# Kernel optimization log

Hardware: AMD Instinct MI355X
Metric: run time of the kernel (lower is better)

## Reference

```python
import jax, jax.numpy as jnp
import numpy as np

DEPTH, C, HS, NH, WS, B = 10, 128, 512, 8, 2, 4096


def _sincos_1d(embed_dim, pos):
    omega = np.arange(embed_dim // 2, dtype=np.float64)
    omega /= embed_dim / 2.0
    omega = 1.0 / 10000 ** omega
    out = np.einsum('m,d->md', pos.reshape(-1), omega)
    return np.concatenate([np.sin(out), np.cos(out)], axis=1)


def _sincos_pos_embed(embed_dim, grid_size):
    g = np.arange(grid_size, dtype=np.float32)
    grid = np.stack(np.meshgrid(g, g), axis=0).reshape(2, -1)
    emb_h = _sincos_1d(embed_dim // 2, grid[0])
    emb_w = _sincos_1d(embed_dim // 2, grid[1])
    return np.concatenate([emb_h, emb_w], axis=1)  # (16, HS)


def _encode_board(x):
    # x: (B,128) int piece ids -> (B,12,8,8) one-hot planes (vectorized encodeBoard)
    x = x.reshape(-1, 2, 8, 8)
    pieces = jnp.arange(1, 7)
    white = (x[:, 0, None, :, :] == pieces[None, :, None, None]).astype(jnp.float32)
    black = (x[:, 1, None, :, :] == pieces[None, :, None, None]).astype(jnp.float32)
    return jnp.concatenate([white, black], axis=1)


def _conv3x3(x, w, b):
    y = jax.lax.conv_general_dilated(x, w, (1, 1), 'SAME',
                                     dimension_numbers=('NCHW', 'OIHW', 'NCHW'))
    return y + b[None, :, None, None]


def _bn(x, g, b, eps=1e-5):
    # training-mode BatchNorm2d: per-batch stats over (N,H,W)
    m = x.mean((0, 2, 3), keepdims=True)
    v = x.var((0, 2, 3), keepdims=True)
    return (x - m) * jax.lax.rsqrt(v + eps) * g[None, :, None, None] + b[None, :, None, None]


def _ln(x, eps=1e-6):
    m = x.mean(-1, keepdims=True)
    v = x.var(-1, keepdims=True)
    return (x - m) * jax.lax.rsqrt(v + eps)


def _window_partition(x, ws):
    b, c, h, w = x.shape
    x = x.reshape(b, c, h // ws, ws, w // ws, ws)
    x = x.transpose(0, 2, 4, 3, 5, 1)  # b h w p1 p2 c
    return x.reshape(b, (h // ws) * (w // ws), ws * ws * c)


def _window_reverse(win, ws, h, w):
    b, n, d = win.shape
    c = d // (ws * ws)
    x = win.reshape(b, h // ws, w // ws, ws, ws, c)
    x = x.transpose(0, 5, 1, 3, 2, 4)  # b c h p1 w p2
    return x.reshape(b, c, h, w)


def _attention(t, qkv_w, qkv_b, proj_w, proj_b):
    b, n, d = t.shape
    hd = d // NH
    qkv = (t @ qkv_w + qkv_b).reshape(b, n, 3, NH, hd)
    q, k, v = jnp.moveaxis(qkv, 2, 0)  # each (b,n,NH,hd)
    attn = jax.nn.softmax(jnp.einsum('bqhd,bkhd->bhqk', q * hd ** -0.5, k), axis=-1)
    out = jnp.einsum('bhqk,bkhd->bqhd', attn, v).reshape(b, n, d)
    return out @ proj_w + proj_b


def _block(x, pos, p):
    (rb1_w, rb1_b, g1, b1, rb2_w, rb2_b, g2, b2,
     qkv_w, qkv_b, proj_w, proj_b, f1_w, f1_b, f2_w, f2_b) = p
    h, w = x.shape[2], x.shape[3]
    z = _bn(_conv3x3(jax.nn.relu(x), rb1_w, rb1_b), g1, b1)
    z = _bn(_conv3x3(jax.nn.relu(z), rb2_w, rb2_b), g2, b2)
    x = x + z
    t = _window_partition(x, WS) + pos
    t = t + _ln(_attention(t, qkv_w, qkv_b, proj_w, proj_b))
    t = t + _ln(jax.nn.relu(t @ f1_w + f1_b) @ f2_w + f2_b)
    return _window_reverse(t, WS, h, w)


def _forward(x, pos_embed, conv1_w, conv1_b, blk, lin1_w, lin1_b, lin2_w, lin2_b):
    h = _conv3x3(_encode_board(x), conv1_w, conv1_b)

    def step(h, p):
        return _block(h, pos_embed, p), None

    h, _ = jax.lax.scan(step, h, blk)
    feat = h.transpose(0, 2, 3, 1).reshape(h.shape[0], -1)  # B (H W C)
    logits = jax.nn.relu(feat @ lin1_w + lin1_b) @ lin2_w + lin2_b
    return jax.nn.softmax(logits, axis=1)


def setup_inputs() -> dict:
    key = jax.random.key(0)
    ks = jax.random.split(key, 16)
    n = lambda k, shp: jax.random.normal(k, shp, dtype=jnp.float32) * 0.02
    inp = {}
    inp['x'] = jax.random.randint(ks[0], (B, 128), 0, 7)
    inp['pos_embed'] = jnp.asarray(_sincos_pos_embed(HS, 8 // WS), dtype=jnp.float32)[None]
    inp['conv1_w'] = n(ks[1], (C, 12, 3, 3))
    inp['conv1_b'] = jnp.zeros((C,), jnp.float32)
    inp['rb1_w'] = n(ks[2], (DEPTH, C, C, 3, 3)); inp['rb1_b'] = jnp.zeros((DEPTH, C), jnp.float32)
    inp['bn1_g'] = jnp.ones((DEPTH, C), jnp.float32); inp['bn1_b'] = jnp.zeros((DEPTH, C), jnp.float32)
    inp['rb2_w'] = n(ks[3], (DEPTH, C, C, 3, 3)); inp['rb2_b'] = jnp.zeros((DEPTH, C), jnp.float32)
    inp['bn2_g'] = jnp.ones((DEPTH, C), jnp.float32); inp['bn2_b'] = jnp.zeros((DEPTH, C), jnp.float32)
    inp['qkv_w'] = n(ks[4], (DEPTH, HS, 3 * HS)); inp['qkv_b'] = jnp.zeros((DEPTH, 3 * HS), jnp.float32)
    inp['proj_w'] = n(ks[5], (DEPTH, HS, HS)); inp['proj_b'] = jnp.zeros((DEPTH, HS), jnp.float32)
    inp['fc1_w'] = n(ks[6], (DEPTH, HS, HS)); inp['fc1_b'] = jnp.zeros((DEPTH, HS), jnp.float32)
    inp['fc2_w'] = n(ks[7], (DEPTH, HS, HS)); inp['fc2_b'] = jnp.zeros((DEPTH, HS), jnp.float32)
    inp['lin1_w'] = n(ks[8], (C * 64, 1024)); inp['lin1_b'] = jnp.zeros((1024,), jnp.float32)
    inp['lin2_w'] = n(ks[9], (1024, 640)); inp['lin2_b'] = jnp.zeros((640,), jnp.float32)
    return inp


def reference(x, pos_embed, conv1_w, conv1_b, rb1_w, rb1_b, bn1_g, bn1_b,
              rb2_w, rb2_b, bn2_g, bn2_b, qkv_w, qkv_b, proj_w, proj_b,
              fc1_w, fc1_b, fc2_w, fc2_b, lin1_w, lin1_b, lin2_w, lin2_b):
    blk = (rb1_w, rb1_b, bn1_g, bn1_b, rb2_w, rb2_b, bn2_g, bn2_b,
           qkv_w, qkv_b, proj_w, proj_b, fc1_w, fc1_b, fc2_w, fc2_b)
    return _forward(x, pos_embed, conv1_w, conv1_b, blk, lin1_w, lin1_b, lin2_w, lin2_b)
```

## Files before the change

### kernel.cpp

```cpp
#include <hip/hip_runtime.h>
#include <hip/hip_fp16.h>
#include <math.h>


#define NBATCH 4096
#define NPOSR  (NBATCH*64)
#define CH     1024
#define CHT    (CH*16)

#define OFF_ACT   0
#define OFF_BIG2  33554432
#define OFF_WT1   (OFF_BIG2 + 16777216)
#define OFF_WTA   (OFF_WT1 + 13824)
#define OFF_WTB   (OFF_WTA + 737280)
#define OFF_WTT   (OFF_WTB + 737280)
#define OFF_STATS (OFF_WTT + 786432)
#define OFF_BIAS  (OFF_STATS + 5120)
#define WS_NEED_FLOATS (OFF_BIAS + 1536)

#define H_QKVB 0
#define H_ATT  25165824
#define H_T2H  8388608
#define H_LOG  8388608

#define T_QKV  0
#define T_PRJ  786432
#define T_F1   1048576
#define T_F2   1310720

typedef _Float16 f16x8 __attribute__((ext_vector_type(8)));
typedef _Float16 f16x4 __attribute__((ext_vector_type(4)));
typedef float f32x4 __attribute__((ext_vector_type(4)));

__device__ inline f32x4 vzero4() { f32x4 z; z[0]=0.f; z[1]=0.f; z[2]=0.f; z[3]=0.f; return z; }

__device__ inline float4 ld_half4(const __half* p) {
  float2 a = __half22float2(*(const __half2*)p);
  float2 b = __half22float2(*(const __half2*)(p + 2));
  return make_float4(a.x, a.y, b.x, b.y);
}

__device__ __forceinline__ void gll16(const void* g, void* lds) {
  __builtin_amdgcn_global_load_lds(
      (__attribute__((address_space(1))) void*)g,
      (__attribute__((address_space(3))) void*)lds,
      16, 0, 0);
}

__global__ void k_zero(float* __restrict__ s) { s[blockIdx.x*256 + threadIdx.x] = 0.f; }

__global__ void k_sentinel(float* __restrict__ out, int n, float val) {
  for (int i = blockIdx.x*blockDim.x + threadIdx.x; i < n; i += gridDim.x*blockDim.x)
    out[i] = val;
}

__global__ __launch_bounds__(256) void k_cvt16(const float* __restrict__ src,
    __half* __restrict__ dst, int n8) {
  int i = blockIdx.x*blockDim.x + threadIdx.x;
  if (i >= n8) return;
  const float4* s4 = (const float4*)&src[i*8];
  float4 v0 = s4[0], v1 = s4[1];
  f16x8 h;
  h[0]=(_Float16)v0.x; h[1]=(_Float16)v0.y; h[2]=(_Float16)v0.z; h[3]=(_Float16)v0.w;
  h[4]=(_Float16)v1.x; h[5]=(_Float16)v1.y; h[6]=(_Float16)v1.z; h[7]=(_Float16)v1.w;
  *(f16x8*)&dst[i*8] = h;
}

__global__ void k_wprep(const float* __restrict__ src, float* __restrict__ dst, int L, int Cin) {
  int total = L * 128 * Cin * 9;
  for (int idx = blockIdx.x*blockDim.x + threadIdx.x; idx < total; idx += gridDim.x*blockDim.x) {
    int kk = idx % 9; int t2 = idx / 9;
    int ci = t2 % Cin; t2 /= Cin;
    int co = t2 % 128; int l  = t2 / 128;
    dst[((size_t)(l*9 + kk)*Cin + ci)*128 + co] = src[idx];
  }
}

__global__ void k_wprep16(const float* __restrict__ src, __half* __restrict__ dst, int L) {
  int total = L * 128 * 128 * 9;
  for (int idx = blockIdx.x*blockDim.x + threadIdx.x; idx < total; idx += gridDim.x*blockDim.x) {
    int kk = idx % 9; int t2 = idx / 9;
    int ci = t2 % 128; t2 /= 128;
    int co = t2 % 128; int l  = t2 / 128;
    dst[((size_t)(l*128 + co))*1152 + kk*128 + ci] = __float2half(src[idx]);
  }
}

__global__ void k_wt16(const float* __restrict__ W, __half* __restrict__ WT, int K, int N) {
  int total = K * N;
  for (int idx = blockIdx.x*blockDim.x + threadIdx.x; idx < total; idx += gridDim.x*blockDim.x) {
    int k = idx / N, n = idx % N;
    WT[(size_t)n*K + k] = __float2half(W[idx]);
  }
}

__global__ void k_wt16x4(const float* __restrict__ Wq, const float* __restrict__ Wp,
                         const float* __restrict__ W1, const float* __restrict__ W2,
                         const float* __restrict__ bq,
                         __half* __restrict__ wTt, float* __restrict__ biasbuf) {
  int gid0 = blockIdx.x*blockDim.x + threadIdx.x;
  if (gid0 < 1536) biasbuf[gid0] = bq[gid0] * (gid0 < 512 ? 0.125f : 1.f);
  const int TOT = 786432 + 3*262144;
  for (int idx = gid0; idx < TOT; idx += gridDim.x*blockDim.x) {
    if (idx < 786432) {
      int k = idx / 1536, n = idx % 1536;
      float v = Wq[idx] * (n < 512 ? 0.125f : 1.f);
      wTt[T_QKV + (size_t)n*512 + k] = __float2half(v);
    } else {
      int r0 = idx - 786432;
      int s = r0 / 262144, r = r0 % 262144;
      int k = r / 512, n = r % 512;
      const float* W = (s == 0) ? Wp : (s == 1) ? W1 : W2;
      wTt[T_PRJ + s*262144 + (size_t)n*512 + k] = __float2half(W[r]);
    }
  }
}

__global__ __launch_bounds__(256) void k_conv1(const int* __restrict__ xin,
    const float* __restrict__ wT1, const float* __restrict__ b1,
    float* __restrict__ out) {
  __shared__ int s_w[64], s_b[64];
  int b = blockIdx.x, t = threadIdx.x;
  if (t < 64) { s_w[t] = xin[b*128 + t]; s_b[t] = xin[b*128 + 64 + t]; }
  __syncthreads();
  int p = t >> 2, i = t & 3;
  int y = p >> 3, x = p & 7;
  float acc[32];
  #pragma unroll
  for (int j = 0; j < 32; ++j) acc[j] = b1[i*32 + j];
  #pragma unroll
  for (int kk = 0; kk < 9; ++kk) {
    int ny = y + kk/3 - 1, nx = x + kk%3 - 1;
    if (ny < 0 || ny > 7 || nx < 0 || nx > 7) continue;
    int np = ny*8 + nx;
    int wp = s_w[np], bp = s_b[np];
    if (wp >= 1 && wp <= 6) {
      const float* w = &wT1[(size_t)(kk*12 + (wp-1))*128 + i*32];
      #pragma unroll
      for (int j = 0; j < 32; ++j) acc[j] += w[j];
    }
    if (bp >= 1 && bp <= 6) {
      const float* w = &wT1[(size_t)(kk*12 + 6 + (bp-1))*128 + i*32];
      #pragma unroll
      for (int j = 0; j < 32; ++j) acc[j] += w[j];
    }
  }
  float* o = &out[((size_t)b*64 + p)*128 + i*32];
  #pragma unroll
  for (int j = 0; j < 8; ++j)
    *(float4*)&o[j*4] = make_float4(acc[j*4], acc[j*4+1], acc[j*4+2], acc[j*4+3]);
}

__device__ inline float cvt_in(float v) { return v; }
__device__ inline float cvt_in(__half v) { return __half2float(v); }

#define IMG_W 136

template<typename TIN>
__global__ __launch_bounds__(256) void k_conv_mfma(const TIN* __restrict__ in,
    const __half* __restrict__ wT , const float* __restrict__ bias,
    const float* __restrict__ stats_in, const float* __restrict__ g,
    const float* __restrict__ bb, int use_bn, __half* __restrict__ out,
    float* __restrict__ stats_out) {
  __shared__ __align__(16) _Float16 s_img[2*65*IMG_W];
  __shared__ __align__(16) _Float16 s_B[2][4096];
  __shared__ float s_sum[128], s_sq[128];
  __shared__ float s_bnp[256];
  int b2 = blockIdx.x, t = threadIdx.x;
  int w = t >> 6, lane = t & 63;

  auto issueB = [&](int win, int buf) {
    #pragma unroll
    for (int i = 0; i < 2; ++i) {
      int rbase = (w*2 + i)*16;
      const __half* g2 = &wT[(size_t)(rbase + (lane>>2))*1152 + win*32 + (lane&3)*8];
      gll16(g2, &s_B[buf][rbase*32]);
    }
  };
  issueB(0, 0);

  if (use_bn && t < 128) {
    const float invN = 1.f / (float)NPOSR;
    float m = stats_in[t] * invN;
    float vv = stats_in[128+t] * invN - m*m;
    float sc = g[t] * rsqrtf(vv + 1e-5f);
    s_bnp[t] = sc;
    s_bnp[128+t] = bb[t] - m*sc;
  }
  __syncthreads();

  for (int idx4 = t; idx4 < 4096; idx4 += 256) {
    int img = idx4 >> 11, rr = (idx4 >> 5) & 63, c4 = (idx4 & 31) * 4;
    const TIN* src = &in[((size_t)(b2*2 + img)*64 + rr)*128 + c4];
    float v0 = cvt_in(src[0]), v1 = cvt_in(src[1]), v2 = cvt_in(src[2]), v3 = cvt_in(src[3]);
    if (use_bn) {
      v0 = s_bnp[c4+0]*v0 + s_bnp[128+c4+0];
      v1 = s_bnp[c4+1]*v1 + s_bnp[128+c4+1];
      v2 = s_bnp[c4+2]*v2 + s_bnp[128+c4+2];
      v3 = s_bnp[c4+3]*v3 + s_bnp[128+c4+3];
    }
    f16x4 h;
    h[0] = (_Float16)fmaxf(v0, 0.f); h[1] = (_Float16)fmaxf(v1, 0.f);
    h[2] = (_Float16)fmaxf(v2, 0.f); h[3] = (_Float16)fmaxf(v3, 0.f);
    *(f16x4*)&s_img[(img*65 + rr)*IMG_W + c4] = h;
  }
  {
    int img = t >> 7, c = t & 127;
    s_img[(img*65 + 64)*IMG_W + c] = (_Float16)0.f;
    if (t < 128) { s_sum[t] = 0.f; s_sq[t] = 0.f; }
  }
  int wm = (w >> 1)*64, wn = (w & 1)*64;
  int fr = lane & 15, fq = lane >> 4;
  int imgo[4], yy[4], xx_[4];
  #pragma unroll
  for (int mt = 0; mt < 4; ++mt) {
    int r = wm + mt*16 + fr;
    imgo[mt] = r >> 6; int p = r & 63; yy[mt] = p >> 3; xx_[mt] = p & 7;
  }
  f32x4 acc[4][4];
  #pragma unroll
  for (int mt = 0; mt < 4; ++mt)
    #pragma unroll
    for (int nt = 0; nt < 4; ++nt) acc[mt][nt] = vzero4();
  __syncthreads();

  #pragma unroll
  for (int kk = 0; kk < 9; ++kk) {
    int dy = kk/3 - 1, dx = kk%3 - 1;
    const _Float16* abase[4];
    #pragma unroll
    for (int mt = 0; mt < 4; ++mt) {
      int ny = yy[mt] + dy, nx = xx_[mt] + dx;
      int row = ((unsigned)ny < 8u && (unsigned)nx < 8u) ? (ny*8 + nx) : 64;
      abase[mt] = &s_img[(imgo[mt]*65 + row)*IMG_W];
    }
    #pragma unroll
    for (int q = 0; q < 4; ++q) {
      int win = kk*4 + q;
      int buf = win & 1;
      if (win + 1 < 36) issueB(win + 1, buf ^ 1);
      f16x8 af[4], bf[4];
      #pragma unroll
      for (int mt = 0; mt < 4; ++mt) af[mt] = *(const f16x8*)&abase[mt][q*32 + fq*8];
      #pragma unroll
      for (int nt = 0; nt < 4; ++nt) bf[nt] = *(const f16x8*)&s_B[buf][(wn + nt*16 + fr)*32 + fq*8];
      #pragma unroll
      for (int mt = 0; mt < 4; ++mt)
        #pragma unroll
        for (int nt = 0; nt < 4; ++nt)
          acc[mt][nt] = __builtin_amdgcn_mfma_f32_16x16x32_f16(af[mt], bf[nt], acc[mt][nt], 0, 0, 0);
      __syncthreads();
    }
  }
  #pragma unroll
  for (int nt = 0; nt < 4; ++nt) {
    int col = wn + nt*16 + fr;
    float bv = bias[col];
    float s = 0.f, q = 0.f;
    #pragma unroll
    for (int mt = 0; mt < 4; ++mt) {
      int rbase = wm + mt*16 + fq*4;
      #pragma unroll
      for (int j = 0; j < 4; ++j) {
        int r = rbase + j;
        int img = r >> 6, p = r & 63;
        float v = acc[mt][nt][j] + bv;
        s += v; q += v*v;
        out[((size_t)(b2*2 + img)*64 + p)*128 + col] = __float2half(v);
      }
    }
    s += __shfl_xor(s, 16); s += __shfl_xor(s, 32);
    q += __shfl_xor(q, 16); q += __shfl_xor(q, 32);
    if (fq == 0) { atomicAdd(&s_sum[col], s); atomicAdd(&s_sq[col], q); }
  }
  __syncthreads();
  if (t < 128) {
    atomicAdd(&stats_out[t], s_sum[t]);
    atomicAdd(&stats_out[128 + t], s_sq[t]);
  }
}

__global__ __launch_bounds__(256) void k_make_t(float* __restrict__ act,
    const __half* __restrict__ z1h, const float* __restrict__ stats_in,
    const float* __restrict__ g, const float* __restrict__ bb,
    const float* __restrict__ pos) {
  __shared__ float s_t[8192];
  __shared__ float s_bnp[256];
  int b = blockIdx.x, t = threadIdx.x;
  if (t < 128) {
    const float invN = 1.f / (float)NPOSR;
    float m = stats_in[t] * invN;
    float vv = stats_in[128+t] * invN - m*m;
    float sc = g[t] * rsqrtf(vv + 1e-5f);
    s_bnp[t] = sc;
    s_bnp[128+t] = bb[t] - m*sc;
  }
  __syncthreads();
  for (int idx4 = t; idx4 < 2048; idx4 += 256) {
    int n = idx4 >> 7, d4 = idx4 & 127;
    int d = d4*4, c = d & 127, q = d >> 7;
    int y = ((n>>2)<<1) + (q>>1), xx = ((n&3)<<1) + (q&1);
    size_t sp = ((size_t)b*64 + y*8 + xx)*128 + c;
    float4 a  = *(const float4*)&act[sp];
    float4 z  = ld_half4(&z1h[sp]);
    float4 sc = *(const float4*)&s_bnp[c];
    float4 sh = *(const float4*)&s_bnp[128+c];
    float4 pe = *(const float4*)&pos[n*512 + d];
    float4 o;
    o.x = a.x + sc.x*z.x + sh.x + pe.x;
    o.y = a.y + sc.y*z.y + sh.y + pe.y;
    o.z = a.z + sc.z*z.z + sh.z + pe.z;
    o.w = a.w + sc.w*z.w + sh.w + pe.w;
    *(float4*)&s_t[n*512 + d] = o;
  }
  __syncthreads();
  for (int idx4 = t; idx4 < 2048; idx4 += 256)
    *(float4*)&act[(size_t)b*8192 + idx4*4] = *(float4*)&s_t[idx4*4];
}

#define QS 1544

__global__ __launch_bounds__(256) void k_attn16(const __half* __restrict__ qkvbuf,
    __half* __restrict__ attnout) {
  __shared__ __align__(16) _Float16 s_qkv[16][QS];
  __shared__ float S[8][16][17];
  int img = blockIdx.x, t = threadIdx.x;
  const __half* src = qkvbuf + (size_t)img*16*1536;
  #pragma unroll
  for (int i = 0; i < 12; ++i) {
    int lin = t + i*256;
    int row = lin / 192, c8 = lin % 192;
    *(f16x8*)&s_qkv[row][c8*8] = *(const f16x8*)&src[(size_t)row*1536 + c8*8];
  }
  __syncthreads();
  {
    int h = t >> 5, qi = (t >> 1) & 15, ko = (t & 1) * 8;
    int rot = t & 31;
    float acc[8];
    #pragma unroll
    for (int k = 0; k < 8; ++k) acc[k] = 0.f;
    const __half2* qr = (const __half2*)&s_qkv[qi][h*64];
    for (int i2 = 0; i2 < 32; ++i2) {
      int d2 = (i2 + rot) & 31;
      float2 q2 = __half22float2(qr[d2]);
      #pragma unroll
      for (int k = 0; k < 8; ++k) {
        float2 k2 = __half22float2(*(const __half2*)&s_qkv[ko + k][512 + h*64 + d2*2]);
        acc[k] += q2.x*k2.x + q2.y*k2.y;
      }
    }
    #pragma unroll
    for (int k = 0; k < 8; ++k) S[h][qi][ko + k] = acc[k];
  }
  __syncthreads();
  if (t < 128) {
    int h = t >> 4, qi = t & 15;
    float* Sr = S[h][qi];
    float mx = -1e30f;
    #pragma unroll
    for (int ki = 0; ki < 16; ++ki) mx = fmaxf(mx, Sr[ki]);
    float sm = 0.f; float e[16];
    #pragma unroll
    for (int ki = 0; ki < 16; ++ki) { e[ki] = expf(Sr[ki] - mx); sm += e[ki]; }
    float inv = 1.f / sm;
    #pragma unroll
    for (int ki = 0; ki < 16; ++ki) Sr[ki] = e[ki]*inv;
  }
  __syncthreads();
  {
    int qi = t >> 4, rem = t & 15;
    int h = rem >> 1, dhb = (rem & 1) * 32;
    int rot = (t >> 2) & 15;
    float P[16];
    #pragma unroll
    for (int k = 0; k < 16; ++k) P[k] = S[h][qi][(k + rot) & 15];
    __half* orow = attnout + ((size_t)img*16 + qi)*512 + h*64 + dhb;
    #pragma unroll
    for (int j = 0; j < 16; ++j) {
      int dh = dhb + 2*j;
      float a0 = 0.f, a1 = 0.f;
      #pragma unroll
      for (int kk2 = 0; kk2 < 16; ++kk2) {
        int ki = (kk2 + rot) & 15;
        float2 v2 = __half22float2(*(const __half2*)&s_qkv[ki][1024 + h*64 + dh]);
        a0 += P[kk2]*v2.x; a1 += P[kk2]*v2.y;
      }
      *(__half2*)&orow[2*j] = __floats2half2_rn(a0, a1);
    }
  }
}

template<int MTI, int NTI, int A16, int B16, int RELU, int OUT16>
__global__ __launch_bounds__(256) void k_mgemm(const void* __restrict__ Ap,
    const void* __restrict__ Bp, const float* __restrict__ bias,
    void* __restrict__ Cp, int M, int N, int K) {
  constexpr int BM = MTI*32;
  constexpr int BN = NTI*32;
  __shared__ __align__(16) _Float16 sA[2][BM*32];
  __shared__ __align__(16) _Float16 sB[2][BN*32];
  int t = threadIdx.x;
  int bm = blockIdx.x * BM, bn = blockIdx.y * BN;
  int w = t >> 6, lane = t & 63;
  int wm = (w >> 1) * (MTI*16), wn = (w & 1) * (NTI*16);
  int fr = lane & 15, fq = lane >> 4;

  auto stageA = [&](int k0, int buf) {
    if (A16) {
      const __half* A = (const __half*)Ap;
      constexpr int NI = MTI/2;
      #pragma unroll
      for (int i = 0; i < NI; ++i) {
        int rbase = (w*NI + i)*16;
        gll16(&A[(size_t)(bm + rbase + (lane>>2))*K + k0 + (lane&3)*8],
              &sA[buf][rbase*32]);
      }
    } else {
      const float* A = (const float*)Ap;
      if (MTI == 4) {
        int srow = t >> 1, skh = (t & 1) * 16;
        const float4* src = (const float4*)&A[(size_t)(bm + srow)*K + k0 + skh];
        float4 v0 = src[0], v1 = src[1], v2 = src[2], v3 = src[3];
        f16x8 h0, h1;
        h0[0]=(_Float16)v0.x; h0[1]=(_Float16)v0.y; h0[2]=(_Float16)v0.z; h0[3]=(_Float16)v0.w;
        h0[4]=(_Float16)v1.x; h0[5]=(_Float16)v1.y; h0[6]=(_Float16)v1.z; h0[7]=(_Float16)v1.w;
        h1[0]=(_Float16)v2.x; h1[1]=(_Float16)v2.y; h1[2]=(_Float16)v2.z; h1[3]=(_Float16)v2.w;
        h1[4]=(_Float16)v3.x; h1[5]=(_Float16)v3.y; h1[6]=(_Float16)v3.z; h1[7]=(_Float16)v3.w;
        *(f16x8*)&sA[buf][srow*32 + skh]     = h0;
        *(f16x8*)&sA[buf][srow*32 + skh + 8] = h1;
      } else {
        int srow = t >> 2, g8 = (t & 3) * 8;
        const float4* src = (const float4*)&A[(size_t)(bm + srow)*K + k0 + g8];
        float4 v0 = src[0], v1 = src[1];
        f16x8 h0;
        h0[0]=(_Float16)v0.x; h0[1]=(_Float16)v0.y; h0[2]=(_Float16)v0.z; h0[3]=(_Float16)v0.w;
        h0[4]=(_Float16)v1.x; h0[5]=(_Float16)v1.y; h0[6]=(_Float16)v1.z; h0[7]=(_Float16)v1.w;
        *(f16x8*)&sA[buf][srow*32 + g8] = h0;
      }
    }
  };
  auto stageB = [&](int k0, int buf) {
    if (B16) {
      const __half* BT = (const __half*)Bp;
      constexpr int NBI = NTI/2;
      #pragma unroll
      for (int i = 0; i < NBI; ++i) {
        int rbase = (w*NBI + i)*16;
        gll16(&BT[(size_t)(bn + rbase + (lane>>2))*K + k0 + (lane&3)*8],
              &sB[buf][rbase*32]);
      }
    } else {
      const float* B = (const float*)Bp;
      int kr = t >> 3, n0 = (t & 7) * 16;
      #pragma unroll
      for (int g = 0; g < 4; ++g) {
        float4 v = *(const float4*)&B[(size_t)(k0 + kr)*N + bn + n0 + g*4];
        sB[buf][(n0+g*4+0)*32 + kr] = (_Float16)v.x;
        sB[buf][(n0+g*4+1)*32 + kr] = (_Float16)v.y;
        sB[buf][(n0+g*4+2)*32 + kr] = (_Float16)v.z;
        sB[buf][(n0+g*4+3)*32 + kr] = (_Float16)v.w;
      }
    }
  };

  f32x4 acc[MTI][NTI];
  #pragma unroll
  for (int mt = 0; mt < MTI; ++mt)
    #pragma unroll
    for (int nt = 0; nt < NTI; ++nt) acc[mt][nt] = vzero4();

  stageA(0, 0); stageB(0, 0);
  __syncthreads();
  int KW = K >> 5;
  for (int kw = 0; kw < KW; ++kw) {
    int buf = kw & 1;
    if (kw + 1 < KW) { stageA((kw+1)*32, buf ^ 1); stageB((kw+1)*32, buf ^ 1); }
    f16x8 af[MTI], bf[NTI];
    #pragma unroll
    for (int mt = 0; mt < MTI; ++mt) af[mt] = *(const f16x8*)&sA[buf][(wm + mt*16 + fr)*32 + fq*8];
    #pragma unroll
    for (int nt = 0; nt < NTI; ++nt) bf[nt] = *(const f16x8*)&sB[buf][(wn + nt*16 + fr)*32 + fq*8];
    #pragma unroll
    for (int mt = 0; mt < MTI; ++mt)
      #pragma unroll
      for (int nt = 0; nt < NTI; ++nt)
        acc[mt][nt] = __builtin_amdgcn_mfma_f32_16x16x32_f16(af[mt], bf[nt], acc[mt][nt], 0, 0, 0);
    __syncthreads();
  }
  #pragma unroll
  for (int mt = 0; mt < MTI; ++mt)
    #pragma unroll
    for (int nt = 0; nt < NTI; ++nt) {
      int col = bn + wn + nt*16 + fr;
      float bv = bias[col];
      #pragma unroll
      for (int j = 0; j < 4; ++j) {
        int row = bm + wm + mt*16 + fq*4 + j;
        float v = acc[mt][nt][j] + bv;
        if (RELU) v = fmaxf(v, 0.f);
        if (OUT16) ((__half*)Cp)[(size_t)row*N + col] = __float2half(v);
        else       ((float*)Cp)[(size_t)row*N + col] = v;
      }
    }
}

__global__ __launch_bounds__(256) void k_lnres(const __half* __restrict__ pout,
    const float* __restrict__ tact, __half* __restrict__ t2h) {
  int t = threadIdx.x;
  int tok = blockIdx.x*4 + (t >> 6);
  int lane = t & 63;
  f16x8 hv = *(const f16x8*)&pout[(size_t)tok*512 + lane*8];
  float v[8]; float s1 = 0.f, s2 = 0.f;
  #pragma unroll
  for (int j = 0; j < 8; ++j) { v[j] = (float)hv[j]; s1 += v[j]; s2 += v[j]*v[j]; }
  #pragma unroll
  for (int m = 32; m >= 1; m >>= 1) { s1 += __shfl_xor(s1, m); s2 += __shfl_xor(s2, m); }
  float mean = s1 * (1.f/512.f);
  float var  = s2 * (1.f/512.f) - mean*mean;
  float rs = rsqrtf(var + 1e-6f);
  const float* ar = &tact[(size_t)tok*512 + lane*8];
  f16x8 o16;
  #pragma unroll
  for (int j = 0; j < 8; ++j) {
    float t2 = ar[j] + (v[j] - mean)*rs;
    o16[j] = (_Float16)t2;
  }
  *(f16x8*)&t2h[(size_t)tok*512 + lane*8] = o16;
}

__global__ __launch_bounds__(256) void k_lnres2(const __half* __restrict__ fout,
    const __half* __restrict__ t2h, float* __restrict__ actimg) {
  __shared__ float s_t2[8192];
  int bimg = blockIdx.x, t = threadIdx.x;
  int lane = t & 63;
  for (int tg = 0; tg < 4; ++tg) {
    int n = tg*4 + (t >> 6);
    size_t row = (size_t)bimg*16 + n;
    f16x8 hv = *(const f16x8*)&fout[row*512 + lane*8];
    float v[8]; float s1 = 0.f, s2 = 0.f;
    #pragma unroll
    for (int j = 0; j < 8; ++j) { v[j] = (float)hv[j]; s1 += v[j]; s2 += v[j]*v[j]; }
    #pragma unroll
    for (int m = 32; m >= 1; m >>= 1) { s1 += __shfl_xor(s1, m); s2 += __shfl_xor(s2, m); }
    float mean = s1 * (1.f/512.f);
    float var  = s2 * (1.f/512.f) - mean*mean;
    float rs = rsqrtf(var + 1e-6f);
    f16x8 tv = *(const f16x8*)&t2h[row*512 + lane*8];
    #pragma unroll
    for (int j = 0; j < 8; ++j)
      s_t2[n*512 + lane*8 + j] = (float)tv[j] + (v[j] - mean)*rs;
  }
  __syncthreads();
  for (int idx = t; idx < 2048; idx += 256) {
    int p = idx >> 5, c = (idx & 31)*4;
    int y = p >> 3, x = p & 7;
    int n = (y >> 1)*4 + (x >> 1);
    int d = ((y & 1)*2 + (x & 1))*128 + c;
    *(float4*)&actimg[(size_t)bimg*8192 + p*128 + c] = *(float4*)&s_t2[n*512 + d];
  }
}

__global__ __launch_bounds__(256) void k_softmax(const float* __restrict__ logits, float* __restrict__ out) {
  int b = blockIdx.x, t = threadIdx.x;
  __shared__ float red[256];
  float m = -1e30f;
  for (int j = t; j < 640; j += 256) m = fmaxf(m, logits[(size_t)b*640 + j]);
  red[t] = m; __syncthreads();
  for (int s = 128; s > 0; s >>= 1) { if (t < s) red[t] = fmaxf(red[t], red[t+s]); __syncthreads(); }
  m = red[0]; __syncthreads();
  float sum = 0.f;
  for (int j = t; j < 640; j += 256) sum += expf(logits[(size_t)b*640 + j] - m);
  red[t] = sum; __syncthreads();
  for (int s = 128; s > 0; s >>= 1) { if (t < s) red[t] += red[t+s]; __syncthreads(); }
  float inv = 1.f / red[0];
  for (int j = t; j < 640; j += 256) out[(size_t)b*640 + j] = expf(logits[(size_t)b*640 + j] - m) * inv;
}

extern "C" void kernel_launch(void* const* d_in, const int* in_sizes, int n_in,
                              void* d_out, int out_size, void* d_ws, size_t ws_size,
                              hipStream_t stream) {
  (void)in_sizes; (void)n_in;
  float* out = (float*)d_out;
  if (ws_size < (size_t)WS_NEED_FLOATS * 4) {
    k_sentinel<<<2048, 256, 0, stream>>>(out, out_size, (float)(ws_size >> 20));
    return;
  }

  const int*   x       = (const int*)d_in[0];
  const float* pos     = (const float*)d_in[1];
  const float* conv1_w = (const float*)d_in[2];
  const float* conv1_b = (const float*)d_in[3];
  const float* rb1_w   = (const float*)d_in[4];
  const float* rb1_b   = (const float*)d_in[5];
  const float* bn1_g   = (const float*)d_in[6];
  const float* bn1_b   = (const float*)d_in[7];
  const float* rb2_w   = (const float*)d_in[8];
  const float* rb2_b   = (const float*)d_in[9];
  const float* bn2_g   = (const float*)d_in[10];
  const float* bn2_b   = (const float*)d_in[11];
  const float* qkv_w   = (const float*)d_in[12];
  const float* qkv_b   = (const float*)d_in[13];
  const float* proj_w  = (const float*)d_in[14];
  const float* proj_b  = (const float*)d_in[15];
  const float* fc1_w   = (const float*)d_in[16];
  const float* fc1_b   = (const float*)d_in[17];
  const float* fc2_w   = (const float*)d_in[18];
  const float* fc2_b   = (const float*)d_in[19];
  const float* lin1_w  = (const float*)d_in[20];
  const float* lin1_b  = (const float*)d_in[21];
  const float* lin2_w  = (const float*)d_in[22];
  const float* lin2_b  = (const float*)d_in[23];

  float*  ws    = (float*)d_ws;
  float*  act   = ws + OFF_ACT;
  __half* big2h = (__half*)(ws + OFF_BIG2);
  float*  wT1   = ws + OFF_WT1;
  __half* wTa16 = (__half*)(ws + OFF_WTA);
  __half* wTb16 = (__half*)(ws + OFF_WTB);
  __half* wTt   = (__half*)(ws + OFF_WTT);
  float*  stats20 = ws + OFF_STATS;
  float*  biasbuf = ws + OFF_BIAS;

  __half* z1h     = big2h;
  __half* qkvbuf  = big2h + H_QKVB;
  __half* attnout = big2h + H_ATT;
  __half* th      = attnout;
  __half* projout = big2h + H_QKVB;
  __half* t2h     = big2h + H_T2H;
  __half* h1      = attnout;
  __half* fc2out  = projout;
  __half* qkvT    = wTt + T_QKV;
  __half* projT   = wTt + T_PRJ;
  __half* fc1T    = wTt + T_F1;
  __half* fc2T    = wTt + T_F2;
  __half* L1h     = big2h;
  float*  logits  = (float*)(big2h + H_LOG);
  __half* lin2T   = wTt;

  k_zero<<<20, 256, 0, stream>>>(stats20);
  k_wprep<<<64, 256, 0, stream>>>(conv1_w, wT1, 1, 12);
  k_wprep16<<<2048, 256, 0, stream>>>(rb1_w, wTa16, 10);
  k_wprep16<<<2048, 256, 0, stream>>>(rb2_w, wTb16, 10);
  k_conv1<<<NBATCH, 256, 0, stream>>>(x, wT1, conv1_b, act);

  for (int l = 0; l < 10; ++l) {
    float* statsA = stats20 + (size_t)(2*l)*256;
    float* statsB = stats20 + (size_t)(2*l + 1)*256;
    k_conv_mfma<float><<<NBATCH/2, 256, 0, stream>>>(act, wTa16 + (size_t)l*147456,
        rb1_b + l*128, (const float*)nullptr, (const float*)nullptr,
        (const float*)nullptr, 0, z1h, statsA);
    k_conv_mfma<__half><<<NBATCH/2, 256, 0, stream>>>(z1h, wTb16 + (size_t)l*147456,
        rb2_b + l*128, statsA, bn1_g + l*128, bn1_b + l*128, 1, z1h, statsB);
    k_make_t<<<NBATCH, 256, 0, stream>>>(act, z1h, statsB, bn2_g + l*128,
        bn2_b + l*128, pos);

    k_wt16x4<<<2048, 256, 0, stream>>>(qkv_w + (size_t)l*786432,
        proj_w + (size_t)l*262144, fc1_w + (size_t)l*262144, fc2_w + (size_t)l*262144,
        qkv_b + l*1536, wTt, biasbuf);

    for (int ch = 0; ch < NBATCH/CH; ++ch) {
      float* tchunk = act + (size_t)ch*CH*8192;
      k_cvt16<<<(CHT*512/8 + 255)/256, 256, 0, stream>>>(tchunk, th, CHT*512/8);
      k_mgemm<4,4,1,1,0,1><<<dim3(CHT/128, 12), 256, 0, stream>>>(th, qkvT,
          biasbuf, qkvbuf, CHT, 1536, 512);
      k_attn16<<<CH, 256, 0, stream>>>(qkvbuf, attnout);
      k_mgemm<4,4,1,1,0,1><<<dim3(CHT/128, 4), 256, 0, stream>>>(attnout, projT,
          proj_b + l*512, projout, CHT, 512, 512);
      k_lnres<<<CHT/4, 256, 0, stream>>>(projout, tchunk, t2h);
      k_mgemm<4,4,1,1,1,1><<<dim3(CHT/128, 4), 256, 0, stream>>>(t2h, fc1T,
          fc1_b + l*512, h1, CHT, 512, 512);
      k_mgemm<4,4,1,1,0,1><<<dim3(CHT/128, 4), 256, 0, stream>>>(h1, fc2T,
          fc2_b + l*512, fc2out, CHT, 512, 512);
      k_lnres2<<<CH, 256, 0, stream>>>(fc2out, t2h, tchunk);
    }
  }
  k_mgemm<2,4,0,0,1,1><<<dim3(4096/64, 8), 256, 0, stream>>>(act, lin1_w, lin1_b, L1h,
      4096, 1024, 8192);
  k_wt16<<<512, 256, 0, stream>>>(lin2_w, lin2T, 1024, 640);
  k_mgemm<2,4,1,1,0,0><<<dim3(4096/64, 5), 256, 0, stream>>>(L1h, lin2T, lin2_b, logits,
      4096, 640, 1024);
  k_softmax<<<NBATCH, 256, 0, stream>>>(logits, out);
}
```

Before: 9.249 ms.

## Store residual activation stream in fp16 instead of fp32

```diff
diff --git a/kernel.cpp b/kernel.cpp
--- a/kernel.cpp
+++ b/kernel.cpp
@@ -9,7 +9,7 @@
 #define CHT    (CH*16)
 
 #define OFF_ACT   0
-#define OFF_BIG2  33554432
+#define OFF_BIG2  16777216
 #define OFF_WT1   (OFF_BIG2 + 16777216)
 #define OFF_WTA   (OFF_WT1 + 13824)
 #define OFF_WTB   (OFF_WTA + 737280)
@@ -40,6 +40,11 @@
   return make_float4(a.x, a.y, b.x, b.y);
 }
 
+__device__ inline void st_half4(__half* p, float4 v) {
+  *(__half2*)p       = __floats2half2_rn(v.x, v.y);
+  *(__half2*)(p + 2) = __floats2half2_rn(v.z, v.w);
+}
+
 __device__ __forceinline__ void gll16(const void* g, void* lds) {
   __builtin_amdgcn_global_load_lds(
       (__attribute__((address_space(1))) void*)g,
@@ -52,18 +57,6 @@
 __global__ void k_sentinel(float* __restrict__ out, int n, float val) {
   for (int i = blockIdx.x*blockDim.x + threadIdx.x; i < n; i += gridDim.x*blockDim.x)
     out[i] = val;
-}
-
-__global__ __launch_bounds__(256) void k_cvt16(const float* __restrict__ src,
-    __half* __restrict__ dst, int n8) {
-  int i = blockIdx.x*blockDim.x + threadIdx.x;
-  if (i >= n8) return;
-  const float4* s4 = (const float4*)&src[i*8];
-  float4 v0 = s4[0], v1 = s4[1];
-  f16x8 h;
-  h[0]=(_Float16)v0.x; h[1]=(_Float16)v0.y; h[2]=(_Float16)v0.z; h[3]=(_Float16)v0.w;
-  h[4]=(_Float16)v1.x; h[5]=(_Float16)v1.y; h[6]=(_Float16)v1.z; h[7]=(_Float16)v1.w;
-  *(f16x8*)&dst[i*8] = h;
 }
 
 __global__ void k_wprep(const float* __restrict__ src, float* __restrict__ dst, int L, int Cin) {
@@ -118,7 +111,7 @@
 
 __global__ __launch_bounds__(256) void k_conv1(const int* __restrict__ xin,
     const float* __restrict__ wT1, const float* __restrict__ b1,
-    float* __restrict__ out) {
+    __half* __restrict__ out) {
   __shared__ int s_w[64], s_b[64];
   int b = blockIdx.x, t = threadIdx.x;
   if (t < 64) { s_w[t] = xin[b*128 + t]; s_b[t] = xin[b*128 + 64 + t]; }
@@ -145,19 +138,15 @@
       for (int j = 0; j < 32; ++j) acc[j] += w[j];
     }
   }
-  float* o = &out[((size_t)b*64 + p)*128 + i*32];
-  #pragma unroll
-  for (int j = 0; j < 8; ++j)
-    *(float4*)&o[j*4] = make_float4(acc[j*4], acc[j*4+1], acc[j*4+2], acc[j*4+3]);
-}
-
-__device__ inline float cvt_in(float v) { return v; }
-__device__ inline float cvt_in(__half v) { return __half2float(v); }
+  __half* o = &out[((size_t)b*64 + p)*128 + i*32];
+  #pragma unroll
+  for (int j = 0; j < 16; ++j)
+    *(__half2*)&o[j*2] = __floats2half2_rn(acc[j*2], acc[j*2+1]);
+}
 
 #define IMG_W 136
 
-template<typename TIN>
-__global__ __launch_bounds__(256) void k_conv_mfma(const TIN* __restrict__ in,
+__global__ __launch_bounds__(256) void k_conv_mfma(const __half* __restrict__ in,
     const __half* __restrict__ wT , const float* __restrict__ bias,
     const float* __restrict__ stats_in, const float* __restrict__ g,
     const float* __restrict__ bb, int use_bn, __half* __restrict__ out,
@@ -191,8 +180,9 @@
 
   for (int idx4 = t; idx4 < 4096; idx4 += 256) {
     int img = idx4 >> 11, rr = (idx4 >> 5) & 63, c4 = (idx4 & 31) * 4;
-    const TIN* src = &in[((size_t)(b2*2 + img)*64 + rr)*128 + c4];
-    float v0 = cvt_in(src[0]), v1 = cvt_in(src[1]), v2 = cvt_in(src[2]), v3 = cvt_in(src[3]);
+    const __half* src = &in[((size_t)(b2*2 + img)*64 + rr)*128 + c4];
+    float4 vv4 = ld_half4(src);
+    float v0 = vv4.x, v1 = vv4.y, v2 = vv4.z, v3 = vv4.w;
     if (use_bn) {
       v0 = s_bnp[c4+0]*v0 + s_bnp[128+c4+0];
       v1 = s_bnp[c4+1]*v1 + s_bnp[128+c4+1];
@@ -280,7 +270,7 @@
   }
 }
 
-__global__ __launch_bounds__(256) void k_make_t(float* __restrict__ act,
+__global__ __launch_bounds__(256) void k_make_t(__half* __restrict__ act,
     const __half* __restrict__ z1h, const float* __restrict__ stats_in,
     const float* __restrict__ g, const float* __restrict__ bb,
     const float* __restrict__ pos) {
@@ -301,7 +291,7 @@
     int d = d4*4, c = d & 127, q = d >> 7;
     int y = ((n>>2)<<1) + (q>>1), xx = ((n&3)<<1) + (q&1);
     size_t sp = ((size_t)b*64 + y*8 + xx)*128 + c;
-    float4 a  = *(const float4*)&act[sp];
+    float4 a  = ld_half4(&act[sp]);
     float4 z  = ld_half4(&z1h[sp]);
     float4 sc = *(const float4*)&s_bnp[c];
     float4 sh = *(const float4*)&s_bnp[128+c];
@@ -314,8 +304,13 @@
     *(float4*)&s_t[n*512 + d] = o;
   }
   __syncthreads();
-  for (int idx4 = t; idx4 < 2048; idx4 += 256)
-    *(float4*)&act[(size_t)b*8192 + idx4*4] = *(float4*)&s_t[idx4*4];
+  for (int idx8 = t; idx8 < 1024; idx8 += 256) {
+    float4 v0 = *(float4*)&s_t[idx8*8];
+    float4 v1 = *(float4*)&s_t[idx8*8 + 4];
+    __half* o = &act[(size_t)b*8192 + idx8*8];
+    st_half4(o, v0);
+    st_half4(o + 4, v1);
+  }
 }
 
 #define QS 1544
@@ -504,7 +499,7 @@
 }
 
 __global__ __launch_bounds__(256) void k_lnres(const __half* __restrict__ pout,
-    const float* __restrict__ tact, __half* __restrict__ t2h) {
+    const __half* __restrict__ tact, __half* __restrict__ t2h) {
   int t = threadIdx.x;
   int tok = blockIdx.x*4 + (t >> 6);
   int lane = t & 63;
@@ -517,18 +512,18 @@
   float mean = s1 * (1.f/512.f);
   float var  = s2 * (1.f/512.f) - mean*mean;
   float rs = rsqrtf(var + 1e-6f);
-  const float* ar = &tact[(size_t)tok*512 + lane*8];
+  f16x8 av = *(const f16x8*)&tact[(size_t)tok*512 + lane*8];
   f16x8 o16;
   #pragma unroll
   for (int j = 0; j < 8; ++j) {
-    float t2 = ar[j] + (v[j] - mean)*rs;
+    float t2 = (float)av[j] + (v[j] - mean)*rs;
     o16[j] = (_Float16)t2;
   }
   *(f16x8*)&t2h[(size_t)tok*512 + lane*8] = o16;
 }
 
 __global__ __launch_bounds__(256) void k_lnres2(const __half* __restrict__ fout,
-    const __half* __restrict__ t2h, float* __restrict__ actimg) {
+    const __half* __restrict__ t2h, __half* __restrict__ actimg) {
   __shared__ float s_t2[8192];
   int bimg = blockIdx.x, t = threadIdx.x;
   int lane = t & 63;
@@ -550,12 +545,16 @@
       s_t2[n*512 + lane*8 + j] = (float)tv[j] + (v[j] - mean)*rs;
   }
   __syncthreads();
-  for (int idx = t; idx < 2048; idx += 256) {
-    int p = idx >> 5, c = (idx & 31)*4;
+  for (int idx = t; idx < 1024; idx += 256) {
+    int p = idx >> 4, c = (idx & 15)*8;
     int y = p >> 3, x = p & 7;
     int n = (y >> 1)*4 + (x >> 1);
     int d = ((y & 1)*2 + (x & 1))*128 + c;
-    *(float4*)&actimg[(size_t)bimg*8192 + p*128 + c] = *(float4*)&s_t2[n*512 + d];
+    float4 v0 = *(float4*)&s_t2[n*512 + d];
+    float4 v1 = *(float4*)&s_t2[n*512 + d + 4];
+    __half* o = &actimg[(size_t)bimg*8192 + p*128 + c];
+    st_half4(o, v0);
+    st_half4(o + 4, v1);
   }
 }
 
@@ -611,7 +610,7 @@
   const float* lin2_b  = (const float*)d_in[23];
 
   float*  ws    = (float*)d_ws;
-  float*  act   = ws + OFF_ACT;
+  __half* act16 = (__half*)(ws + OFF_ACT);
   __half* big2h = (__half*)(ws + OFF_BIG2);
   float*  wT1   = ws + OFF_WT1;
   __half* wTa16 = (__half*)(ws + OFF_WTA);
@@ -623,7 +622,6 @@
   __half* z1h     = big2h;
   __half* qkvbuf  = big2h + H_QKVB;
   __half* attnout = big2h + H_ATT;
-  __half* th      = attnout;
   __half* projout = big2h + H_QKVB;
   __half* t2h     = big2h + H_T2H;
   __half* h1      = attnout;
@@ -640,17 +638,17 @@
   k_wprep<<<64, 256, 0, stream>>>(conv1_w, wT1, 1, 12);
   k_wprep16<<<2048, 256, 0, stream>>>(rb1_w, wTa16, 10);
   k_wprep16<<<2048, 256, 0, stream>>>(rb2_w, wTb16, 10);
-  k_conv1<<<NBATCH, 256, 0, stream>>>(x, wT1, conv1_b, act);
+  k_conv1<<<NBATCH, 256, 0, stream>>>(x, wT1, conv1_b, act16);
 
   for (int l = 0; l < 10; ++l) {
     float* statsA = stats20 + (size_t)(2*l)*256;
     float* statsB = stats20 + (size_t)(2*l + 1)*256;
-    k_conv_mfma<float><<<NBATCH/2, 256, 0, stream>>>(act, wTa16 + (size_t)l*147456,
+    k_conv_mfma<<<NBATCH/2, 256, 0, stream>>>(act16, wTa16 + (size_t)l*147456,
         rb1_b + l*128, (const float*)nullptr, (const float*)nullptr,
         (const float*)nullptr, 0, z1h, statsA);
-    k_conv_mfma<__half><<<NBATCH/2, 256, 0, stream>>>(z1h, wTb16 + (size_t)l*147456,
+    k_conv_mfma<<<NBATCH/2, 256, 0, stream>>>(z1h, wTb16 + (size_t)l*147456,
         rb2_b + l*128, statsA, bn1_g + l*128, bn1_b + l*128, 1, z1h, statsB);
-    k_make_t<<<NBATCH, 256, 0, stream>>>(act, z1h, statsB, bn2_g + l*128,
+    k_make_t<<<NBATCH, 256, 0, stream>>>(act16, z1h, statsB, bn2_g + l*128,
         bn2_b + l*128, pos);
 
     k_wt16x4<<<2048, 256, 0, stream>>>(qkv_w + (size_t)l*786432,
@@ -658,9 +656,8 @@
         qkv_b + l*1536, wTt, biasbuf);
 
     for (int ch = 0; ch < NBATCH/CH; ++ch) {
-      float* tchunk = act + (size_t)ch*CH*8192;
-      k_cvt16<<<(CHT*512/8 + 255)/256, 256, 0, stream>>>(tchunk, th, CHT*512/8);
-      k_mgemm<4,4,1,1,0,1><<<dim3(CHT/128, 12), 256, 0, stream>>>(th, qkvT,
+      __half* tchunk = act16 + (size_t)ch*CH*8192;
+      k_mgemm<4,4,1,1,0,1><<<dim3(CHT/128, 12), 256, 0, stream>>>(tchunk, qkvT,
           biasbuf, qkvbuf, CHT, 1536, 512);
       k_attn16<<<CH, 256, 0, stream>>>(qkvbuf, attnout);
       k_mgemm<4,4,1,1,0,1><<<dim3(CHT/128, 4), 256, 0, stream>>>(attnout, projT,
@@ -673,7 +670,7 @@
       k_lnres2<<<CH, 256, 0, stream>>>(fc2out, t2h, tchunk);
     }
   }
-  k_mgemm<2,4,0,0,1,1><<<dim3(4096/64, 8), 256, 0, stream>>>(act, lin1_w, lin1_b, L1h,
+  k_mgemm<2,4,1,0,1,1><<<dim3(4096/64, 8), 256, 0, stream>>>(act16, lin1_w, lin1_b, L1h,
       4096, 1024, 8192);
   k_wt16<<<512, 256, 0, stream>>>(lin2_w, lin2T, 1024, 640);
   k_mgemm<2,4,1,1,0,0><<<dim3(4096/64, 5), 256, 0, stream>>>(L1h, lin2T, lin2_b, logits,
```

After: 8.449 ms (median of 2 runs). -8.7%, faster.
